# Kernel tuning notes

Hardware: AMD Instinct MI355X
Metric: run time of the kernel (lower is better)

## Reference

```python
import jax, jax.numpy as jnp
import numpy as np

LMAX = 5
NUMCOLS = [512, 512, 512, 512, 512, 512]
EPS = 1e-05
CNT = 1.0
BATCH = 1024


def setup_inputs() -> dict:
    key = jax.random.key(0)
    keys = jax.random.split(key, 2 * (LMAX + 1))
    inp = {}
    for l in range(LMAX + 1):
        inp[f"f{l}"] = jax.random.normal(
            keys[l], (BATCH, NUMCOLS[l], 2 * l + 1, 2), dtype=jnp.float32
        )
    # running stds, initialized like init='debug' (np.random.seed(0) rand)
    rng = np.random.RandomState(0)
    std_flat = rng.rand(int(np.sum(NUMCOLS))).astype(np.float32)
    st = 0
    for l in range(LMAX + 1):
        inp[f"stds{l}"] = jnp.asarray(std_flat[st : st + NUMCOLS[l]])
        st += NUMCOLS[l]
    return inp


def _norm_one(fl, std_l):
    # fl: [B, C, M, 2]; std_l: [C]
    norm = jnp.sqrt(jnp.sum(fl * fl, axis=3))          # [B, C, M]
    batch_std = jnp.std(norm, axis=(0, 2))             # [C], population std (ddof=0) like np.std
    new_std = std_l * (CNT / (CNT + 1.0)) + batch_std / (CNT + 1.0)
    scale = jnp.maximum(EPS, new_std)[None, :, None, None]
    return fl / scale


def reference(f0, f1, f2, f3, f4, f5, stds0, stds1, stds2, stds3, stds4, stds5):
    fs = [f0, f1, f2, f3, f4, f5]
    stds = [stds0, stds1, stds2, stds3, stds4, stds5]
    return tuple(_norm_one(fl, st) for fl, st in zip(fs, stds))
```

## Files before the change

kernel.cpp:

```cpp
#include <hip/hip_runtime.h>

#define NB_C 512
#define NB_B 1024
#define SB_RED 32
#define SB_NRM 32

typedef float vf4 __attribute__((ext_vector_type(4)));

__device__ __forceinline__ int decode_lw(int wl, int& w) {
  if (wl < 1)  { w = wl;      return 0; }
  if (wl < 4)  { w = wl - 1;  return 1; }
  if (wl < 9)  { w = wl - 4;  return 2; }
  if (wl < 16) { w = wl - 9;  return 3; }
  if (wl < 25) { w = wl - 16; return 4; }
  w = wl - 25; return 5;
}

__device__ __forceinline__ const vf4* pick_f(int l,
    const vf4* f0, const vf4* f1, const vf4* f2,
    const vf4* f3, const vf4* f4, const vf4* f5) {
  switch (l) {
    case 0: return f0; case 1: return f1; case 2: return f2;
    case 3: return f3; case 4: return f4; default: return f5;
  }
}

__device__ __forceinline__ const float* pick_s(int l,
    const float* s0, const float* s1, const float* s2,
    const float* s3, const float* s4, const float* s5) {
  switch (l) {
    case 0: return s0; case 1: return s1; case 2: return s2;
    case 3: return s3; case 4: return s4; default: return s5;
  }
}

__global__ __launch_bounds__(256)
void bn_reduce(const vf4* __restrict__ f0, const vf4* __restrict__ f1,
               const vf4* __restrict__ f2, const vf4* __restrict__ f3,
               const vf4* __restrict__ f4, const vf4* __restrict__ f5,
               float* __restrict__ gsum, float* __restrict__ gsq)
{
  const int bs = blockIdx.x % SB_RED;
  const int wl = blockIdx.x / SB_RED;
  int w; const int l = decode_lw(wl, w);
  const int M = 2 * l + 1;
  const vf4* __restrict__ f = pick_f(l, f0, f1, f2, f3, f4, f5);

  const int t  = threadIdx.x;
  const int o4 = w * 256 + t;
  const int e0 = 2 * o4;
  const int c0 = e0 / M;
  const int c1 = (e0 + 1) / M;
  const int rs4 = 256 * M;
  const int Bc  = NB_B / SB_RED;

  const vf4* p = f + (size_t)(bs * Bc) * rs4 + o4;
  float s0 = 0.f, q0 = 0.f, s1 = 0.f, q1 = 0.f;
#pragma unroll 8
  for (int i = 0; i < Bc; ++i) {
    vf4 v = p[(size_t)i * rs4];
    float r0 = v.x * v.x + v.y * v.y;
    float r1 = v.z * v.z + v.w * v.w;
    s0 += sqrtf(r0); q0 += r0;
    s1 += sqrtf(r1); q1 += r1;
  }

  __shared__ float ls[512];
  __shared__ float lq[512];
  __shared__ short lc[512];
  ls[2*t]   = s0; lq[2*t]   = q0; lc[2*t]   = (short)c0;
  ls[2*t+1] = s1; lq[2*t+1] = q1; lc[2*t+1] = (short)c1;
  __syncthreads();

  const int base = l * NB_C;
#pragma unroll
  for (int k = 0; k < 2; ++k) {
    const int e = 2 * t + k;
    const short c = lc[e];
    if (e == 0 || lc[e-1] != c) {
      float a = 0.f, a2 = 0.f;
      int j = e;
      while (j < 512 && lc[j] == c) { a += ls[j]; a2 += lq[j]; ++j; }
      atomicAdd(&gsum[base + (int)c], a);
      atomicAdd(&gsq [base + (int)c], a2);
    }
  }
}

__device__ __forceinline__ float chan_scale(float sum, float sq, float rstd,
                                            float cnt) {
  const float mean = sum / cnt;
  const float var  = fmaxf(sq / cnt - mean * mean, 0.f);
  const float bstd = sqrtf(var);
  const float nstd = 0.5f * (rstd + bstd);
  return 1.0f / fmaxf(1e-5f, nstd);
}

__global__ __launch_bounds__(256)
void bn_norm(const vf4* __restrict__ f0, const vf4* __restrict__ f1,
             const vf4* __restrict__ f2, const vf4* __restrict__ f3,
             const vf4* __restrict__ f4, const vf4* __restrict__ f5,
             const float* __restrict__ s0, const float* __restrict__ s1,
             const float* __restrict__ s2, const float* __restrict__ s3,
             const float* __restrict__ s4, const float* __restrict__ s5,
             const float* __restrict__ gsum, const float* __restrict__ gsq,
             vf4* __restrict__ out)
{
  const int bs = blockIdx.x % SB_NRM;
  const int wl = blockIdx.x / SB_NRM;
  int w; const int l = decode_lw(wl, w);
  const int cumM = wl - w;
  const int M = 2 * l + 1;
  const vf4* __restrict__ f = pick_f(l, f0, f1, f2, f3, f4, f5);
  const float* __restrict__ sp = pick_s(l, s0, s1, s2, s3, s4, s5);

  const int t  = threadIdx.x;
  const int o4 = w * 256 + t;
  const int e0 = 2 * o4;
  const int c0 = e0 / M;
  const int c1 = (e0 + 1) / M;
  const int base = l * NB_C;
  const float cnt = (float)(NB_B * M);
  const float sc0 = chan_scale(gsum[base + c0], gsq[base + c0], sp[c0], cnt);
  const float sc1 = chan_scale(gsum[base + c1], gsq[base + c1], sp[c1], cnt);
  const int rs4 = 256 * M;
  const int Bc  = NB_B / SB_NRM;

  const size_t ob = (size_t)262144 * cumM;
  const size_t tb = (size_t)(bs * Bc) * rs4 + o4;
  const vf4* p = f + tb;
  vf4* q = out + ob + tb;
#pragma unroll 8
  for (int i = 0; i < Bc; ++i) {
    vf4 v = p[(size_t)i * rs4];
    v.x *= sc0; v.y *= sc0; v.z *= sc1; v.w *= sc1;
    __builtin_nontemporal_store(v, &q[(size_t)i * rs4]);
  }
}

extern "C" void kernel_launch(void* const* d_in, const int* in_sizes, int n_in,
                              void* d_out, int out_size, void* d_ws, size_t ws_size,
                              hipStream_t stream) {
  const vf4* f[6];
  const float* s[6];
  for (int l = 0; l < 6; ++l) {
    f[l] = (const vf4*)d_in[l];
    s[l] = (const float*)d_in[6 + l];
  }
  float* gsum = (float*)d_ws;
  float* gsq  = gsum + 6 * NB_C;

  (void)hipMemsetAsync(gsum, 0, 2 * 6 * NB_C * sizeof(float), stream);

  bn_reduce<<<36 * SB_RED, 256, 0, stream>>>(
      f[0], f[1], f[2], f[3], f[4], f[5], gsum, gsq);
  bn_norm<<<36 * SB_NRM, 256, 0, stream>>>(
      f[0], f[1], f[2], f[3], f[4], f[5],
      s[0], s[1], s[2], s[3], s[4], s[5],
      gsum, gsq, (vf4*)d_out);
}
```

Measured before the change: 81.72 us.

## Fuse reduce and normalize kernels with a grid-wide atomic barrier

Merges the statistics-reduction and normalization kernels into one persistent kernel of 576 blocks that sync through a global atomic counter barrier, then read the channel sums with coherent loads. This removes one kernel launch and lets the second pass re-read data that may still sit in the L2/MALL cache. It also halves the batch split per block (SB 32 to 16). In exchange it relies on every block being co-resident, since otherwise the spin barrier could deadlock, and the spin-wait adds its own cost.

```diff
diff --git a/kernel.cpp b/kernel.cpp
--- a/kernel.cpp
+++ b/kernel.cpp
@@ -2,8 +2,8 @@
 
 #define NB_C 512
 #define NB_B 1024
-#define SB_RED 32
-#define SB_NRM 32
+#define SB   16
+#define GRID (36 * SB)
 
 typedef float vf4 __attribute__((ext_vector_type(4)));
 
@@ -34,17 +34,27 @@
   }
 }
 
-__global__ __launch_bounds__(256)
-void bn_reduce(const vf4* __restrict__ f0, const vf4* __restrict__ f1,
-               const vf4* __restrict__ f2, const vf4* __restrict__ f3,
-               const vf4* __restrict__ f4, const vf4* __restrict__ f5,
-               float* __restrict__ gsum, float* __restrict__ gsq)
+__device__ __forceinline__ float coh_load(const float* p) {
+  return __hip_atomic_load(p, __ATOMIC_RELAXED, __HIP_MEMORY_SCOPE_AGENT);
+}
+
+__global__ __launch_bounds__(256, 6)
+void bn_fused(const vf4* __restrict__ f0, const vf4* __restrict__ f1,
+              const vf4* __restrict__ f2, const vf4* __restrict__ f3,
+              const vf4* __restrict__ f4, const vf4* __restrict__ f5,
+              const float* __restrict__ s0, const float* __restrict__ s1,
+              const float* __restrict__ s2, const float* __restrict__ s3,
+              const float* __restrict__ s4, const float* __restrict__ s5,
+              float* __restrict__ gsum, float* __restrict__ gsq,
+              unsigned int* __restrict__ bar, vf4* __restrict__ out)
 {
-  const int bs = blockIdx.x % SB_RED;
-  const int wl = blockIdx.x / SB_RED;
+  const int bs = blockIdx.x % SB;
+  const int wl = blockIdx.x / SB;
   int w; const int l = decode_lw(wl, w);
+  const int cumM = wl - w;
   const int M = 2 * l + 1;
   const vf4* __restrict__ f = pick_f(l, f0, f1, f2, f3, f4, f5);
+  const float* __restrict__ sp = pick_s(l, s0, s1, s2, s3, s4, s5);
 
   const int t  = threadIdx.x;
   const int o4 = w * 256 + t;
@@ -52,24 +62,26 @@
   const int c0 = e0 / M;
   const int c1 = (e0 + 1) / M;
   const int rs4 = 256 * M;
-  const int Bc  = NB_B / SB_RED;
+  const int Bc  = NB_B / SB;
 
-  const vf4* p = f + (size_t)(bs * Bc) * rs4 + o4;
-  float s0 = 0.f, q0 = 0.f, s1 = 0.f, q1 = 0.f;
+  const size_t tb = (size_t)(bs * Bc) * rs4 + o4;
+  const vf4* p = f + tb;
+
+  float sa0 = 0.f, qa0 = 0.f, sa1 = 0.f, qa1 = 0.f;
 #pragma unroll 8
   for (int i = 0; i < Bc; ++i) {
     vf4 v = p[(size_t)i * rs4];
     float r0 = v.x * v.x + v.y * v.y;
     float r1 = v.z * v.z + v.w * v.w;
-    s0 += sqrtf(r0); q0 += r0;
-    s1 += sqrtf(r1); q1 += r1;
+    sa0 += sqrtf(r0); qa0 += r0;
+    sa1 += sqrtf(r1); qa1 += r1;
   }
 
   __shared__ float ls[512];
   __shared__ float lq[512];
   __shared__ short lc[512];
-  ls[2*t]   = s0; lq[2*t]   = q0; lc[2*t]   = (short)c0;
-  ls[2*t+1] = s1; lq[2*t+1] = q1; lc[2*t+1] = (short)c1;
+  ls[2*t]   = sa0; lq[2*t]   = qa0; lc[2*t]   = (short)c0;
+  ls[2*t+1] = sa1; lq[2*t+1] = qa1; lc[2*t+1] = (short)c1;
   __syncthreads();
 
   const int base = l * NB_C;
@@ -85,51 +97,31 @@
       atomicAdd(&gsq [base + (int)c], a2);
     }
   }
-}
 
-__device__ __forceinline__ float chan_scale(float sum, float sq, float rstd,
-                                            float cnt) {
-  const float mean = sum / cnt;
-  const float var  = fmaxf(sq / cnt - mean * mean, 0.f);
-  const float bstd = sqrtf(var);
-  const float nstd = 0.5f * (rstd + bstd);
-  return 1.0f / fmaxf(1e-5f, nstd);
-}
+  __syncthreads();
+  __threadfence();
+  if (t == 0) {
+    __hip_atomic_fetch_add(bar, 1u, __ATOMIC_ACQ_REL, __HIP_MEMORY_SCOPE_AGENT);
+    while (__hip_atomic_load(bar, __ATOMIC_ACQUIRE, __HIP_MEMORY_SCOPE_AGENT)
+           < (unsigned int)GRID) {
+      __builtin_amdgcn_s_sleep(2);
+    }
+  }
+  __syncthreads();
 
-__global__ __launch_bounds__(256)
-void bn_norm(const vf4* __restrict__ f0, const vf4* __restrict__ f1,
-             const vf4* __restrict__ f2, const vf4* __restrict__ f3,
-             const vf4* __restrict__ f4, const vf4* __restrict__ f5,
-             const float* __restrict__ s0, const float* __restrict__ s1,
-             const float* __restrict__ s2, const float* __restrict__ s3,
-             const float* __restrict__ s4, const float* __restrict__ s5,
-             const float* __restrict__ gsum, const float* __restrict__ gsq,
-             vf4* __restrict__ out)
-{
-  const int bs = blockIdx.x % SB_NRM;
-  const int wl = blockIdx.x / SB_NRM;
-  int w; const int l = decode_lw(wl, w);
-  const int cumM = wl - w;
-  const int M = 2 * l + 1;
-  const vf4* __restrict__ f = pick_f(l, f0, f1, f2, f3, f4, f5);
-  const float* __restrict__ sp = pick_s(l, s0, s1, s2, s3, s4, s5);
+  const float cnt = (float)(NB_B * M);
+  const float rc = 1.0f / cnt;
+  float sum0 = coh_load(&gsum[base + c0]);
+  float sq0  = coh_load(&gsq [base + c0]);
+  float sum1 = coh_load(&gsum[base + c1]);
+  float sq1  = coh_load(&gsq [base + c1]);
+  float m0 = sum0 * rc, m1 = sum1 * rc;
+  float bstd0 = sqrtf(fmaxf(sq0 * rc - m0 * m0, 0.f));
+  float bstd1 = sqrtf(fmaxf(sq1 * rc - m1 * m1, 0.f));
+  const float sc0 = 1.0f / fmaxf(1e-5f, 0.5f * (sp[c0] + bstd0));
+  const float sc1 = 1.0f / fmaxf(1e-5f, 0.5f * (sp[c1] + bstd1));
 
-  const int t  = threadIdx.x;
-  const int o4 = w * 256 + t;
-  const int e0 = 2 * o4;
-  const int c0 = e0 / M;
-  const int c1 = (e0 + 1) / M;
-  const int base = l * NB_C;
-  const float cnt = (float)(NB_B * M);
-  const float sc0 = chan_scale(gsum[base + c0], gsq[base + c0], sp[c0], cnt);
-  const float sc1 = chan_scale(gsum[base + c1], gsq[base + c1], sp[c1], cnt);
-  const int rs4 = 256 * M;
-  const int Bc  = NB_B / SB_NRM;
-
-  const size_t ob = (size_t)262144 * cumM;
-  const size_t tb = (size_t)(bs * Bc) * rs4 + o4;
-  const vf4* p = f + tb;
-  vf4* q = out + ob + tb;
+  vf4* q = out + (size_t)262144 * cumM + tb;
 #pragma unroll 8
   for (int i = 0; i < Bc; ++i) {
     vf4 v = p[(size_t)i * rs4];
@@ -149,13 +141,12 @@
   }
   float* gsum = (float*)d_ws;
   float* gsq  = gsum + 6 * NB_C;
+  unsigned int* bar = (unsigned int*)(gsq + 6 * NB_C);
 
-  (void)hipMemsetAsync(gsum, 0, 2 * 6 * NB_C * sizeof(float), stream);
+  (void)hipMemsetAsync(d_ws, 0, 6160 * sizeof(float), stream);
 
-  bn_reduce<<<36 * SB_RED, 256, 0, stream>>>(
-      f[0], f[1], f[2], f[3], f[4], f[5], gsum, gsq);
-  bn_norm<<<36 * SB_NRM, 256, 0, stream>>>(
+  bn_fused<<<GRID, 256, 0, stream>>>(
       f[0], f[1], f[2], f[3], f[4], f[5],
       s[0], s[1], s[2], s[3], s[4], s[5],
-      gsum, gsq, (vf4*)d_out);
+      gsum, gsq, bar, (vf4*)d_out);
 }
```

Result: slower. 179.1 us (+119.1%).
